# Kernel tuning notes

Hardware: AMD Instinct MI355X
Metric: run time of the kernel (lower is better)

The kernel has to match this reference:

```python
import jax, jax.numpy as jnp
import numpy as np
from jax import lax

B_SZ = 64
D_MODEL = 768
D_INNER = 1536   # expand * d_model
D_STATE = 16
D_CONV = 4
DT_RANK = 48     # ceil(768/16)
ROWS, COLS = 16, 16
L = ROWS * COLS
LN_EPS = 1e-5


def setup_inputs() -> dict:
    key = jax.random.key(0)
    ks = jax.random.split(key, 16)
    def nrm(k, shape, s):
        return jax.random.normal(k, shape, jnp.float32) * s
    # A_log init as in Mamba: log(arange(1..d_state)) tiled over d_inner
    A_log = jnp.log(jnp.tile(jnp.arange(1, D_STATE + 1, dtype=jnp.float32)[None, :], (D_INNER, 1)))
    # dt bias init: inverse-softplus of dt ~ LogUniform(1e-3, 1e-1)
    def dt_bias_init(k):
        u = jax.random.uniform(k, (D_INNER,), jnp.float32)
        dt = jnp.exp(u * (np.log(0.1) - np.log(0.001)) + np.log(0.001))
        return dt + jnp.log(-jnp.expm1(-dt))
    dt_std = DT_RANK ** -0.5
    return {
        "hidden_states": jax.random.normal(ks[0], (B_SZ, L, D_MODEL), jnp.float32),
        "in_proj_w": nrm(ks[1], (2 * D_INNER, D_MODEL), 0.02),
        "conv_w": nrm(ks[2], (D_INNER, D_CONV), 0.2),
        "conv_bias": nrm(ks[3], (D_INNER,), 0.1),
        "conv_w_b": nrm(ks[4], (D_INNER, D_CONV), 0.2),
        "conv_bias_b": nrm(ks[5], (D_INNER,), 0.1),
        "x_proj_w": nrm(ks[6], (DT_RANK + 2 * D_STATE, D_INNER), 0.02),
        "x_proj_w_b": nrm(ks[7], (DT_RANK + 2 * D_STATE, D_INNER), 0.02),
        "dt_proj_w": jax.random.uniform(ks[8], (D_INNER, DT_RANK), jnp.float32, -dt_std, dt_std),
        "dt_proj_w_b": jax.random.uniform(ks[9], (D_INNER, DT_RANK), jnp.float32, -dt_std, dt_std),
        "dt_bias": dt_bias_init(ks[10]),
        "dt_bias_b": dt_bias_init(ks[11]),
        "A_log": A_log,
        "A_b_log": A_log,
        "Dp": jnp.ones((D_INNER,), jnp.float32),
        "Dp_b": jnp.ones((D_INNER,), jnp.float32),
        "ln_gamma": jnp.ones((D_INNER,), jnp.float32),
        "ln_beta": jnp.zeros((D_INNER,), jnp.float32),
        "out_proj_w": nrm(ks[12], (D_MODEL, D_INNER), 0.02),
    }


def _causal_conv_silu(x, w, b):
    # x: (B, D, L); depthwise causal conv (left-pad K-1) + SiLU
    y = lax.conv_general_dilated(x, w[:, None, :], (1,), [(D_CONV - 1, 0)],
                                 dimension_numbers=("NCH", "OIH", "NCH"),
                                 feature_group_count=D_INNER)
    return jax.nn.silu(y + b[None, :, None])


def _selective_scan(u, dt, A_log, Bm, Cm, dt_bias):
    # u, dt: (B, D, Lr); Bm, Cm: (B, N, Lr)
    A = -jnp.exp(A_log)                                     # (D, N)
    delta = jax.nn.softplus(dt + dt_bias[None, :, None])    # (B, D, Lr)
    dA = jnp.exp(jnp.einsum("bdl,dn->lbdn", delta, A))     # (Lr, B, D, N)
    dBu = jnp.einsum("bdl,bnl,bdl->lbdn", delta, Bm, u)    # (Lr, B, D, N)
    C_l = jnp.moveaxis(Cm, -1, 0)                           # (Lr, B, N)
    def step(h, inp):
        dA_t, dBu_t, C_t = inp
        h = dA_t * h + dBu_t
        return h, jnp.einsum("bdn,bn->bd", h, C_t)
    h0 = jnp.zeros(dA.shape[1:], dA.dtype)
    _, ys = lax.scan(step, h0, (dA, dBu, C_l))
    return jnp.moveaxis(ys, 0, -1)                          # (B, D, Lr)


def _direction(x, conv_w, conv_bias, x_proj_w, dt_proj_w, dt_bias, A_log, Dp):
    xc = _causal_conv_silu(x, conv_w, conv_bias)            # (B, D, L)
    x_comp = xc.reshape(-1, D_INNER, ROWS, COLS).mean(axis=3)  # (B, D, ROWS)
    x_dbl = jnp.einsum("bdl,ed->ble", x_comp, x_proj_w)    # (B, ROWS, R+2N)
    dt, Bm, Cm = jnp.split(x_dbl, [DT_RANK, DT_RANK + D_STATE], axis=-1)
    dt = jnp.einsum("blr,dr->bdl", dt, dt_proj_w)          # (B, D, ROWS)
    Bm = jnp.moveaxis(Bm, 1, 2)                             # (B, N, ROWS)
    Cm = jnp.moveaxis(Cm, 1, 2)
    y = _selective_scan(x_comp, dt, A_log, Bm, Cm, dt_bias)
    return jnp.repeat(y, COLS, axis=2) + Dp[None, :, None] * xc  # (B, D, L)


def reference(hidden_states, in_proj_w, conv_w, conv_bias, conv_w_b, conv_bias_b,
              x_proj_w, x_proj_w_b, dt_proj_w, dt_proj_w_b, dt_bias, dt_bias_b,
              A_log, A_b_log, Dp, Dp_b, ln_gamma, ln_beta, out_proj_w):
    xz = jnp.einsum("bld,ed->bel", hidden_states, in_proj_w)  # (B, 2*Di, L)
    x, z = jnp.split(xz, 2, axis=1)
    out_f = _direction(x, conv_w, conv_bias, x_proj_w, dt_proj_w, dt_bias, A_log, Dp)
    out_b = _direction(x[:, :, ::-1], conv_w_b, conv_bias_b, x_proj_w_b, dt_proj_w_b, dt_bias_b, A_b_log, Dp_b)
    comb = jnp.moveaxis((out_f + out_b[:, :, ::-1]) * 0.5, 1, 2)  # (B, L, Di)
    mu = comb.mean(-1, keepdims=True)
    var = comb.var(-1, keepdims=True)
    normed = (comb - mu) * lax.rsqrt(var + LN_EPS) * ln_gamma + ln_beta
    gated = normed * jax.nn.silu(jnp.moveaxis(z, 1, 2))
    return jnp.einsum("bld,od->blo", gated, out_proj_w)       # (B, L, d_model)
```

## Files before the change

kernel.cpp:

```cpp
#include <hip/hip_runtime.h>
#include <cstdint>
#include <cstddef>

typedef __bf16 bf16_t;
typedef __attribute__((ext_vector_type(2))) __bf16 bf16x2;
typedef __attribute__((ext_vector_type(8))) __bf16 bf16x8;
typedef __attribute__((ext_vector_type(4))) float f32x4;

#define NB     64
#define LSEQ   256
#define DM     768
#define DI     1536
#define NSTATE 16
#define NROWS  16
#define RANK   48

#define BF16_PROBE 0x3F803F80u

__device__ __forceinline__ float bf2f(bf16_t v) { return (float)v; }

__device__ __forceinline__ float ldp(const void* p, size_t i, bool isbf) {
  return isbf ? (float)((const bf16_t*)p)[i] : ((const float*)p)[i];
}

__device__ __forceinline__ float silu_f(float x) {
  const float e = __expf(-fabsf(x));
  return (x >= 0.f) ? (x / (1.f + e)) : (x * e / (1.f + e));
}

__device__ __forceinline__ void async16(const bf16_t* g, bf16_t* l) {
  __builtin_amdgcn_global_load_lds(
      (const __attribute__((address_space(1))) void*)g,
      (__attribute__((address_space(3))) void*)l, 16, 0, 0);
}

__global__ __launch_bounds__(256) void cvt_kernel(
    const void* __restrict__ in, bf16_t* __restrict__ out, int n8,
    const uint32_t* __restrict__ probe)
{
  const int i = blockIdx.x * 256 + threadIdx.x;
  if (i >= n8) return;
  if (probe[0] == BF16_PROBE) {
    ((bf16x8*)out)[i] = ((const bf16x8*)in)[i];
  } else {
    const float* f = (const float*)in + (size_t)i * 8;
    f32x4 lo = *(const f32x4*)f, hi = *(const f32x4*)(f + 4);
    ((bf16x8*)out)[i] = (bf16x8){(bf16_t)lo.x, (bf16_t)lo.y, (bf16_t)lo.z, (bf16_t)lo.w,
                                 (bf16_t)hi.x, (bf16_t)hi.y, (bf16_t)hi.z, (bf16_t)hi.w};
  }
}

__global__ __launch_bounds__(256) void gemm_bt_kernel(
    const bf16_t* __restrict__ A, const bf16_t* __restrict__ B,
    void* __restrict__ C, int M, int N, int K, int cIsF32)
{
  __shared__ bf16_t As[128 * 64];
  __shared__ bf16_t Bs[128 * 64];
  const int tid  = threadIdx.x;
  const int wave = tid >> 6;
  const int lane = tid & 63;
  const size_t bm = (size_t)blockIdx.y * 128;
  const size_t bn = (size_t)blockIdx.x * 128;
  const int wm = (wave >> 1) * 64;
  const int wn = (wave & 1) * 64;

  const int src_rr  = lane >> 3;
  const int src_col = ((lane & 7) ^ src_rr) * 8;

  f32x4 acc[4][4];
#pragma unroll
  for (int i = 0; i < 4; i++)
#pragma unroll
    for (int j = 0; j < 4; j++) acc[i][j] = (f32x4){0.f, 0.f, 0.f, 0.f};

  for (int k0 = 0; k0 < K; k0 += 64) {
#pragma unroll
    for (int j = 0; j < 4; j++) {
      const int c = wave * 4 + j;
      const size_t row = c * 8 + src_rr;
      async16(A + (bm + row) * (size_t)K + k0 + src_col, &As[c * 512]);
      async16(B + (bn + row) * (size_t)K + k0 + src_col, &Bs[c * 512]);
    }
    __syncthreads();
#pragma unroll
    for (int s = 0; s < 2; s++) {
      const int r    = lane & 15;
      const int quad = lane >> 4;
      const int r7   = lane & 7;
      const int slot = ((s * 4 + quad) ^ r7) * 8;
      bf16x8 af[4], bfr[4];
#pragma unroll
      for (int mt = 0; mt < 4; mt++)
        af[mt] = *(const bf16x8*)&As[(wm + mt * 16 + r) * 64 + slot];
#pragma unroll
      for (int nt = 0; nt < 4; nt++)
        bfr[nt] = *(const bf16x8*)&Bs[(wn + nt * 16 + r) * 64 + slot];
#pragma unroll
      for (int mt = 0; mt < 4; mt++)
#pragma unroll
        for (int nt = 0; nt < 4; nt++)
          acc[mt][nt] = __builtin_amdgcn_mfma_f32_16x16x32_bf16(
              af[mt], bfr[nt], acc[mt][nt], 0, 0, 0);
    }
    __syncthreads();
  }

  const int col = lane & 15;
  const int rb  = (lane >> 4) * 4;
#pragma unroll
  for (int mt = 0; mt < 4; mt++)
#pragma unroll
    for (int nt = 0; nt < 4; nt++)
#pragma unroll
      for (int r = 0; r < 4; r++) {
        const size_t m = bm + wm + mt * 16 + rb + r;
        const size_t n = bn + wn + nt * 16 + col;
        const size_t ci = m * (size_t)N + n;
        if (cIsF32) ((float*)C)[ci] = acc[mt][nt][r];
        else        ((bf16_t*)C)[ci] = (bf16_t)acc[mt][nt][r];
      }
}

__global__ __launch_bounds__(256) void conv_kernel(
    const bf16_t* __restrict__ xz,
    const void* __restrict__ cw_f, const void* __restrict__ cb_f,
    const void* __restrict__ cw_b, const void* __restrict__ cb_b,
    bf16_t* __restrict__ xc_f, bf16_t* __restrict__ xc_b,
    float* __restrict__ comp_f, float* __restrict__ comp_b,
    const uint32_t* __restrict__ probe)
{
  const bool isbf = (probe[0] == BF16_PROBE);
  const int dir = blockIdx.y;
  int bi = blockIdx.x;
  const int chunk = bi & 3;
  bi >>= 2;
  const int b = bi / 3;
  const int pblk = bi % 3;
  const int d0 = (pblk * 256 + threadIdx.x) * 2;
  const void* cw = dir ? cw_b : cw_f;
  const void* cb = dir ? cb_b : cb_f;
  bf16_t* xc = dir ? xc_b : xc_f;
  float* comp = dir ? comp_b : comp_f;

  const float w00 = ldp(cw, d0 * 4 + 0, isbf), w01 = ldp(cw, d0 * 4 + 1, isbf),
              w02 = ldp(cw, d0 * 4 + 2, isbf), w03 = ldp(cw, d0 * 4 + 3, isbf);
  const float w10 = ldp(cw, (d0 + 1) * 4 + 0, isbf), w11 = ldp(cw, (d0 + 1) * 4 + 1, isbf),
              w12 = ldp(cw, (d0 + 1) * 4 + 2, isbf), w13 = ldp(cw, (d0 + 1) * 4 + 3, isbf);
  const float bias0 = ldp(cb, d0, isbf), bias1 = ldp(cb, d0 + 1, isbf);

  float a3 = 0.f, a2 = 0.f, a1 = 0.f;
  float c3 = 0.f, c2 = 0.f, c1 = 0.f;
  const int lr0 = chunk * 64;
  if (lr0 >= 3) {
#pragma unroll
    for (int i = 3; i >= 1; --i) {
      const int lrp = lr0 - i;
      const int l = dir ? (LSEQ - 1 - lrp) : lrp;
      bf16x2 xv = *(const bf16x2*)(xz + ((size_t)b * LSEQ + l) * (2 * DI) + d0);
      a3 = a2; a2 = a1; a1 = (float)xv.x;
      c3 = c2; c2 = c1; c1 = (float)xv.y;
    }
  }

  float s0 = 0.f, s1 = 0.f;
  for (int lr = lr0; lr < lr0 + 64; ++lr) {
    const int l = dir ? (LSEQ - 1 - lr) : lr;
    bf16x2 xv = *(const bf16x2*)(xz + ((size_t)b * LSEQ + l) * (2 * DI) + d0);
    const float x0 = (float)xv.x, x1 = (float)xv.y;
    float y0 = silu_f(bias0 + w00 * a3 + w01 * a2 + w02 * a1 + w03 * x0);
    float y1 = silu_f(bias1 + w10 * c3 + w11 * c2 + w12 * c1 + w13 * x1);
    a3 = a2; a2 = a1; a1 = x0;
    c3 = c2; c2 = c1; c1 = x1;
    *(bf16x2*)(xc + ((size_t)b * LSEQ + lr) * DI + d0) = (bf16x2){(bf16_t)y0, (bf16_t)y1};
    s0 += y0; s1 += y1;
    if ((lr & 15) == 15) {
      size_t ci = ((size_t)b * NROWS + (lr >> 4)) * DI + d0;
      comp[ci]     = s0 * (1.f / 16.f);
      comp[ci + 1] = s1 * (1.f / 16.f);
      s0 = 0.f; s1 = 0.f;
    }
  }
}

__global__ __launch_bounds__(256) void xproj_kernel(
    const float* __restrict__ comp_f, const float* __restrict__ comp_b,
    const void* __restrict__ w_f, const void* __restrict__ w_b,
    float* __restrict__ xd_f, float* __restrict__ xd_b,
    const uint32_t* __restrict__ probe)
{
  const bool isbf = (probe[0] == BF16_PROBE);
  const int dir = blockIdx.y;
  const int row = blockIdx.x;
  const float* comp = dir ? comp_b : comp_f;
  const void* W = dir ? w_b : w_f;
  float* out = dir ? xd_b : xd_f;

  __shared__ float xrow[DI];
  for (int i = threadIdx.x; i < DI; i += 256) xrow[i] = comp[(size_t)row * DI + i];
  __syncthreads();

  const int wave = threadIdx.x >> 6, lane = threadIdx.x & 63;
  for (int oo = 0; oo < 20; ++oo) {
    const int o = wave * 20 + oo;
    float s = 0.f;
#pragma unroll
    for (int j = 0; j < 24; ++j) {
      const int k = lane + 64 * j;
      s += xrow[k] * ldp(W, (size_t)o * DI + k, isbf);
    }
    for (int off = 32; off; off >>= 1) s += __shfl_down(s, off);
    if (lane == 0) out[(size_t)row * 80 + o] = s;
  }
}

__global__ __launch_bounds__(256) void scan_kernel(
    const float* __restrict__ xd_fg, const float* __restrict__ xd_bg,
    const float* comp_f, const float* comp_b,
    const void* __restrict__ dtw_f, const void* __restrict__ dtw_b,
    const void* __restrict__ dtb_f, const void* __restrict__ dtb_b,
    const void* __restrict__ Al_f, const void* __restrict__ Al_b,
    float* y_fg, float* y_bg,
    const uint32_t* __restrict__ probe)
{
  const bool isbf = (probe[0] == BF16_PROBE);
  const int dir = blockIdx.y;
  const int b = blockIdx.x / 6;
  const int d = (blockIdx.x % 6) * 256 + threadIdx.x;
  const float* xd_g = dir ? xd_bg : xd_fg;
  const float* comp = dir ? comp_b : comp_f;
  const void* dtw = dir ? dtw_b : dtw_f;
  const void* dtb = dir ? dtb_b : dtb_f;
  const void* Al  = dir ? Al_b : Al_f;
  float* y = dir ? y_bg : y_fg;

  __shared__ float xd[NROWS * 80];
  for (int i = threadIdx.x; i < NROWS * 80; i += 256) xd[i] = xd_g[(size_t)b * (NROWS * 80) + i];
  __syncthreads();

  float dt[NROWS];
#pragma unroll
  for (int l = 0; l < NROWS; l++) dt[l] = 0.f;
  for (int r = 0; r < RANK; r++) {
    const float w = ldp(dtw, (size_t)d * RANK + r, isbf);
#pragma unroll
    for (int l = 0; l < NROWS; l++) dt[l] += xd[l * 80 + r] * w;
  }

  float A[NSTATE];
#pragma unroll
  for (int n = 0; n < NSTATE; n++) A[n] = -__expf(ldp(Al, (size_t)d * NSTATE + n, isbf));
  const float bias = ldp(dtb, d, isbf);

  float h[NSTATE];
#pragma unroll
  for (int n = 0; n < NSTATE; n++) h[n] = 0.f;

  for (int l = 0; l < NROWS; l++) {
    const float u = comp[((size_t)b * NROWS + l) * DI + d];
    const float dv = dt[l] + bias;
    const float delta = (dv > 15.f) ? dv : log1pf(__expf(dv));
    const float du = delta * u;
    float yv = 0.f;
#pragma unroll
    for (int n = 0; n < NSTATE; n++) {
      const float hn = __expf(delta * A[n]) * h[n] + du * xd[l * 80 + RANK + n];
      h[n] = hn;
      yv += hn * xd[l * 80 + RANK + NSTATE + n];
    }
    y[((size_t)b * NROWS + l) * DI + d] = yv;
  }
}

__global__ __launch_bounds__(256) void combine_kernel(
    const float* __restrict__ y_f, const float* __restrict__ y_b,
    bf16_t* xcg_f,
    const bf16_t* __restrict__ xc_b,
    const bf16_t* __restrict__ xz,
    const void* __restrict__ Dp, const void* __restrict__ Dp_b,
    const void* __restrict__ gamma, const void* __restrict__ beta,
    const uint32_t* __restrict__ probe)
{
  const bool isbf = (probe[0] == BF16_PROBE);
  const int m = blockIdx.x;
  const int b = m >> 8, l = m & 255;
  const int lr = LSEQ - 1 - l;
  const int tid = threadIdx.x;

  float v[6];
  float sum = 0.f, sq = 0.f;
#pragma unroll
  for (int i = 0; i < 6; i++) {
    const int d = tid + i * 256;
    const float cf = bf2f(xcg_f[((size_t)b * LSEQ + l) * DI + d]);
    const float cb = bf2f(xc_b[((size_t)b * LSEQ + lr) * DI + d]);
    const float vf = y_f[((size_t)b * NROWS + (l >> 4)) * DI + d] + ldp(Dp, d, isbf) * cf;
    const float vb = y_b[((size_t)b * NROWS + (lr >> 4)) * DI + d] + ldp(Dp_b, d, isbf) * cb;
    const float c = 0.5f * (vf + vb);
    v[i] = c; sum += c; sq += c * c;
  }
  for (int off = 32; off; off >>= 1) {
    sum += __shfl_down(sum, off);
    sq  += __shfl_down(sq, off);
  }
  __shared__ float rs[4], rq[4];
  if ((tid & 63) == 0) { rs[tid >> 6] = sum; rq[tid >> 6] = sq; }
  __syncthreads();
  const float S  = rs[0] + rs[1] + rs[2] + rs[3];
  const float SQ = rq[0] + rq[1] + rq[2] + rq[3];
  const float mu = S * (1.f / (float)DI);
  const float var = fmaxf(SQ * (1.f / (float)DI) - mu * mu, 0.f);
  const float rstd = rsqrtf(var + 1e-5f);
#pragma unroll
  for (int i = 0; i < 6; i++) {
    const int d = tid + i * 256;
    const float nrm = (v[i] - mu) * rstd * ldp(gamma, d, isbf) + ldp(beta, d, isbf);
    const float z = bf2f(xz[((size_t)b * LSEQ + l) * (2 * DI) + DI + d]);
    xcg_f[(size_t)m * DI + d] = (bf16_t)(nrm * silu_f(z));
  }
}

extern "C" void kernel_launch(void* const* d_in, const int* in_sizes, int n_in,
                              void* d_out, int out_size, void* d_ws, size_t ws_size,
                              hipStream_t stream)
{
  (void)in_sizes; (void)n_in; (void)out_size; (void)ws_size;
  const void* H     = d_in[0];
  const void* Win   = d_in[1];
  const void* cw_f  = d_in[2];
  const void* cb_f  = d_in[3];
  const void* cw_b  = d_in[4];
  const void* cb_b  = d_in[5];
  const void* xpw_f = d_in[6];
  const void* xpw_b = d_in[7];
  const void* dtw_f = d_in[8];
  const void* dtw_b = d_in[9];
  const void* dtb_f = d_in[10];
  const void* dtb_b = d_in[11];
  const void* Al_f  = d_in[12];
  const void* Al_b  = d_in[13];
  const void* Dp    = d_in[14];
  const void* Dp_b  = d_in[15];
  const void* gam   = d_in[16];
  const void* bet   = d_in[17];
  const void* Wout  = d_in[18];
  const uint32_t* probe = (const uint32_t*)d_in[14];

  const size_t M = (size_t)NB * LSEQ;
  char* ws = (char*)d_ws;
  bf16_t* xz    = (bf16_t*)ws;  ws += M * (2 * DI) * sizeof(bf16_t);
  bf16_t* xc_f  = (bf16_t*)ws;  ws += M * DI * sizeof(bf16_t);
  bf16_t* xc_b  = (bf16_t*)ws;  ws += M * DI * sizeof(bf16_t);
  float* comp_f = (float*)ws;   ws += (size_t)NB * NROWS * DI * sizeof(float);
  float* comp_b = (float*)ws;   ws += (size_t)NB * NROWS * DI * sizeof(float);
  float* xd_f   = (float*)ws;   ws += (size_t)NB * NROWS * 80 * sizeof(float);
  float* xd_b   = (float*)ws;   ws += (size_t)NB * NROWS * 80 * sizeof(float);
  bf16_t* Hb    = (bf16_t*)ws;  ws += M * DM * sizeof(bf16_t);
  bf16_t* Winb  = (bf16_t*)ws;  ws += (size_t)(2 * DI) * DM * sizeof(bf16_t);
  bf16_t* Woutb = (bf16_t*)ws;  ws += (size_t)DM * DI * sizeof(bf16_t);

  cvt_kernel<<<(int)((M * DM / 8 + 255) / 256), 256, 0, stream>>>(H, Hb, (int)(M * DM / 8), probe);
  cvt_kernel<<<(2 * DI * DM / 8 + 255) / 256, 256, 0, stream>>>(Win, Winb, 2 * DI * DM / 8, probe);
  cvt_kernel<<<(DM * DI / 8 + 255) / 256, 256, 0, stream>>>(Wout, Woutb, DM * DI / 8, probe);

  gemm_bt_kernel<<<dim3(2 * DI / 128, M / 128), 256, 0, stream>>>(
      Hb, Winb, xz, (int)M, 2 * DI, DM, 0);

  conv_kernel<<<dim3(768, 2), 256, 0, stream>>>(
      xz, cw_f, cb_f, cw_b, cb_b, xc_f, xc_b, comp_f, comp_b, probe);

  xproj_kernel<<<dim3(NB * NROWS, 2), 256, 0, stream>>>(
      comp_f, comp_b, xpw_f, xpw_b, xd_f, xd_b, probe);

  scan_kernel<<<dim3(NB * (DI / 256), 2), 256, 0, stream>>>(
      xd_f, xd_b, comp_f, comp_b, dtw_f, dtw_b, dtb_f, dtb_b, Al_f, Al_b,
      comp_f, comp_b, probe);

  combine_kernel<<<dim3(NB * LSEQ), 256, 0, stream>>>(
      comp_f, comp_b, xc_f, xc_b, xz, Dp, Dp_b, gam, bet, probe);

  gemm_bt_kernel<<<dim3(DM / 128, M / 128), 256, 0, stream>>>(
      xc_f, Woutb, d_out, (int)M, DM, DI, 1);
}
```

Baseline: 517.0 us.

## Use 256x128 GEMM tile for in_proj, merge conv directions, vectorize combine

Adds a 256x128-tile GEMM for the input projection, doubling per-wave M work (8x4 MFMA tiles) to raise operand reuse from LDS and halve B-tile reloads. The conv kernel now handles both forward and backward directions in one block, reusing the same xz rows from cache instead of launching a second grid. The combine kernel switches to paired bf16x2/float2 loads and stores. The larger tile increases register pressure (128 accumulator floats per lane) and LDS use, and it halves the GEMM grid, which may reduce occupancy.

```diff
diff --git a/kernel.cpp b/kernel.cpp
--- a/kernel.cpp
+++ b/kernel.cpp
@@ -6,6 +6,7 @@
 typedef __attribute__((ext_vector_type(2))) __bf16 bf16x2;
 typedef __attribute__((ext_vector_type(8))) __bf16 bf16x8;
 typedef __attribute__((ext_vector_type(4))) float f32x4;
+typedef __attribute__((ext_vector_type(2))) float f32x2;
 
 #define NB     64
 #define LSEQ   256
@@ -85,9 +86,7 @@
 #pragma unroll
     for (int s = 0; s < 2; s++) {
       const int r    = lane & 15;
-      const int quad = lane >> 4;
-      const int r7   = lane & 7;
-      const int slot = ((s * 4 + quad) ^ r7) * 8;
+      const int slot = ((s * 4 + (lane >> 4)) ^ (lane & 7)) * 8;
       bf16x8 af[4], bfr[4];
 #pragma unroll
       for (int mt = 0; mt < 4; mt++)
@@ -118,6 +117,78 @@
         const size_t ci = m * (size_t)N + n;
         if (cIsF32) ((float*)C)[ci] = acc[mt][nt][r];
         else        ((bf16_t*)C)[ci] = (bf16_t)acc[mt][nt][r];
+      }
+}
+
+__global__ __launch_bounds__(256) void gemm_bt_256(
+    const bf16_t* __restrict__ A, const bf16_t* __restrict__ B,
+    bf16_t* __restrict__ C, int M, int N, int K)
+{
+  __shared__ bf16_t As[256 * 64];
+  __shared__ bf16_t Bs[128 * 64];
+  const int tid  = threadIdx.x;
+  const int wave = tid >> 6;
+  const int lane = tid & 63;
+  const size_t bm = (size_t)blockIdx.y * 256;
+  const size_t bn = (size_t)blockIdx.x * 128;
+  const int wm = (wave >> 1) * 128;
+  const int wn = (wave & 1) * 64;
+
+  const int src_rr  = lane >> 3;
+  const int src_col = ((lane & 7) ^ src_rr) * 8;
+
+  f32x4 acc[8][4];
+#pragma unroll
+  for (int i = 0; i < 8; i++)
+#pragma unroll
+    for (int j = 0; j < 4; j++) acc[i][j] = (f32x4){0.f, 0.f, 0.f, 0.f};
+
+  for (int k0 = 0; k0 < K; k0 += 64) {
+#pragma unroll
+    for (int j = 0; j < 8; j++) {
+      const int c = wave * 8 + j;
+      const size_t row = c * 8 + src_rr;
+      async16(A + (bm + row) * (size_t)K + k0 + src_col, &As[c * 512]);
+    }
+#pragma unroll
+    for (int j = 0; j < 4; j++) {
+      const int c = wave * 4 + j;
+      const size_t row = c * 8 + src_rr;
+      async16(B + (bn + row) * (size_t)K + k0 + src_col, &Bs[c * 512]);
+    }
+    __syncthreads();
+#pragma unroll
+    for (int s = 0; s < 2; s++) {
+      const int r    = lane & 15;
+      const int slot = ((s * 4 + (lane >> 4)) ^ (lane & 7)) * 8;
+      bf16x8 af[8], bfr[4];
+#pragma unroll
+      for (int mt = 0; mt < 8; mt++)
+        af[mt] = *(const bf16x8*)&As[(wm + mt * 16 + r) * 64 + slot];
+#pragma unroll
+      for (int nt = 0; nt < 4; nt++)
+        bfr[nt] = *(const bf16x8*)&Bs[(wn + nt * 16 + r) * 64 + slot];
+#pragma unroll
+      for (int mt = 0; mt < 8; mt++)
+#pragma unroll
+        for (int nt = 0; nt < 4; nt++)
+          acc[mt][nt] = __builtin_amdgcn_mfma_f32_16x16x32_bf16(
+              af[mt], bfr[nt], acc[mt][nt], 0, 0, 0);
+    }
+    __syncthreads();
+  }
+
+  const int col = lane & 15;
+  const int rb  = (lane >> 4) * 4;
+#pragma unroll
+  for (int mt = 0; mt < 8; mt++)
+#pragma unroll
+    for (int nt = 0; nt < 4; nt++)
+#pragma unroll
+      for (int r = 0; r < 4; r++) {
+        const size_t m = bm + wm + mt * 16 + rb + r;
+        const size_t n = bn + wn + nt * 16 + col;
+        C[m * (size_t)N + n] = (bf16_t)acc[mt][nt][r];
       }
 }
 
@@ -130,54 +201,83 @@
     const uint32_t* __restrict__ probe)
 {
   const bool isbf = (probe[0] == BF16_PROBE);
-  const int dir = blockIdx.y;
   int bi = blockIdx.x;
   const int chunk = bi & 3;
   bi >>= 2;
   const int b = bi / 3;
   const int pblk = bi % 3;
   const int d0 = (pblk * 256 + threadIdx.x) * 2;
-  const void* cw = dir ? cw_b : cw_f;
-  const void* cb = dir ? cb_b : cb_f;
-  bf16_t* xc = dir ? xc_b : xc_f;
-  float* comp = dir ? comp_b : comp_f;
-
-  const float w00 = ldp(cw, d0 * 4 + 0, isbf), w01 = ldp(cw, d0 * 4 + 1, isbf),
-              w02 = ldp(cw, d0 * 4 + 2, isbf), w03 = ldp(cw, d0 * 4 + 3, isbf);
-  const float w10 = ldp(cw, (d0 + 1) * 4 + 0, isbf), w11 = ldp(cw, (d0 + 1) * 4 + 1, isbf),
-              w12 = ldp(cw, (d0 + 1) * 4 + 2, isbf), w13 = ldp(cw, (d0 + 1) * 4 + 3, isbf);
-  const float bias0 = ldp(cb, d0, isbf), bias1 = ldp(cb, d0 + 1, isbf);
-
-  float a3 = 0.f, a2 = 0.f, a1 = 0.f;
-  float c3 = 0.f, c2 = 0.f, c1 = 0.f;
-  const int lr0 = chunk * 64;
-  if (lr0 >= 3) {
-#pragma unroll
-    for (int i = 3; i >= 1; --i) {
-      const int lrp = lr0 - i;
-      const int l = dir ? (LSEQ - 1 - lrp) : lrp;
-      bf16x2 xv = *(const bf16x2*)(xz + ((size_t)b * LSEQ + l) * (2 * DI) + d0);
-      a3 = a2; a2 = a1; a1 = (float)xv.x;
-      c3 = c2; c2 = c1; c1 = (float)xv.y;
-    }
-  }
-
-  float s0 = 0.f, s1 = 0.f;
-  for (int lr = lr0; lr < lr0 + 64; ++lr) {
-    const int l = dir ? (LSEQ - 1 - lr) : lr;
-    bf16x2 xv = *(const bf16x2*)(xz + ((size_t)b * LSEQ + l) * (2 * DI) + d0);
-    const float x0 = (float)xv.x, x1 = (float)xv.y;
-    float y0 = silu_f(bias0 + w00 * a3 + w01 * a2 + w02 * a1 + w03 * x0);
-    float y1 = silu_f(bias1 + w10 * c3 + w11 * c2 + w12 * c1 + w13 * x1);
-    a3 = a2; a2 = a1; a1 = x0;
-    c3 = c2; c2 = c1; c1 = x1;
-    *(bf16x2*)(xc + ((size_t)b * LSEQ + lr) * DI + d0) = (bf16x2){(bf16_t)y0, (bf16_t)y1};
-    s0 += y0; s1 += y1;
-    if ((lr & 15) == 15) {
-      size_t ci = ((size_t)b * NROWS + (lr >> 4)) * DI + d0;
-      comp[ci]     = s0 * (1.f / 16.f);
-      comp[ci + 1] = s1 * (1.f / 16.f);
-      s0 = 0.f; s1 = 0.f;
+
+  const float fw00 = ldp(cw_f, d0 * 4 + 0, isbf), fw01 = ldp(cw_f, d0 * 4 + 1, isbf),
+              fw02 = ldp(cw_f, d0 * 4 + 2, isbf), fw03 = ldp(cw_f, d0 * 4 + 3, isbf);
+  const float fw10 = ldp(cw_f, (d0 + 1) * 4 + 0, isbf), fw11 = ldp(cw_f, (d0 + 1) * 4 + 1, isbf),
+              fw12 = ldp(cw_f, (d0 + 1) * 4 + 2, isbf), fw13 = ldp(cw_f, (d0 + 1) * 4 + 3, isbf);
+  const float fb0 = ldp(cb_f, d0, isbf), fb1 = ldp(cb_f, d0 + 1, isbf);
+  const float bw00 = ldp(cw_b, d0 * 4 + 0, isbf), bw01 = ldp(cw_b, d0 * 4 + 1, isbf),
+              bw02 = ldp(cw_b, d0 * 4 + 2, isbf), bw03 = ldp(cw_b, d0 * 4 + 3, isbf);
+  const float bw10 = ldp(cw_b, (d0 + 1) * 4 + 0, isbf), bw11 = ldp(cw_b, (d0 + 1) * 4 + 1, isbf),
+              bw12 = ldp(cw_b, (d0 + 1) * 4 + 2, isbf), bw13 = ldp(cw_b, (d0 + 1) * 4 + 3, isbf);
+  const float bb0 = ldp(cb_b, d0, isbf), bb1 = ldp(cb_b, d0 + 1, isbf);
+
+  const size_t rowbase = (size_t)b * LSEQ;
+  const int l0 = chunk * 64;
+
+  {
+    float a3 = 0.f, a2 = 0.f, a1 = 0.f, c3 = 0.f, c2 = 0.f, c1 = 0.f;
+    if (l0 >= 3) {
+#pragma unroll
+      for (int i = 3; i >= 1; --i) {
+        bf16x2 xv = *(const bf16x2*)(xz + (rowbase + l0 - i) * (2 * DI) + d0);
+        a3 = a2; a2 = a1; a1 = (float)xv.x;
+        c3 = c2; c2 = c1; c1 = (float)xv.y;
+      }
+    }
+    float s0 = 0.f, s1 = 0.f;
+    for (int l = l0; l < l0 + 64; ++l) {
+      bf16x2 xv = *(const bf16x2*)(xz + (rowbase + l) * (2 * DI) + d0);
+      const float x0 = (float)xv.x, x1 = (float)xv.y;
+      float y0 = silu_f(fb0 + fw00 * a3 + fw01 * a2 + fw02 * a1 + fw03 * x0);
+      float y1 = silu_f(fb1 + fw10 * c3 + fw11 * c2 + fw12 * c1 + fw13 * x1);
+      a3 = a2; a2 = a1; a1 = x0;
+      c3 = c2; c2 = c1; c1 = x1;
+      *(bf16x2*)(xc_f + (rowbase + l) * DI + d0) = (bf16x2){(bf16_t)y0, (bf16_t)y1};
+      s0 += y0; s1 += y1;
+      if ((l & 15) == 15) {
+        size_t ci = ((size_t)b * NROWS + (l >> 4)) * DI + d0;
+        comp_f[ci]     = s0 * (1.f / 16.f);
+        comp_f[ci + 1] = s1 * (1.f / 16.f);
+        s0 = 0.f; s1 = 0.f;
+      }
+    }
+  }
+
+  {
+    float a3 = 0.f, a2 = 0.f, a1 = 0.f, c3 = 0.f, c2 = 0.f, c1 = 0.f;
+    if (chunk < 3) {
+#pragma unroll
+      for (int i = 3; i >= 1; --i) {
+        bf16x2 xv = *(const bf16x2*)(xz + (rowbase + l0 + 63 + i) * (2 * DI) + d0);
+        a3 = a2; a2 = a1; a1 = (float)xv.x;
+        c3 = c2; c2 = c1; c1 = (float)xv.y;
+      }
+    }
+    float s0 = 0.f, s1 = 0.f;
+    for (int s = l0 + 63; s >= l0; --s) {
+      const int lr = LSEQ - 1 - s;
+      bf16x2 xv = *(const bf16x2*)(xz + (rowbase + s) * (2 * DI) + d0);
+      const float x0 = (float)xv.x, x1 = (float)xv.y;
+      float y0 = silu_f(bb0 + bw00 * a3 + bw01 * a2 + bw02 * a1 + bw03 * x0);
+      float y1 = silu_f(bb1 + bw10 * c3 + bw11 * c2 + bw12 * c1 + bw13 * x1);
+      a3 = a2; a2 = a1; a1 = x0;
+      c3 = c2; c2 = c1; c1 = x1;
+      *(bf16x2*)(xc_b + (rowbase + lr) * DI + d0) = (bf16x2){(bf16_t)y0, (bf16_t)y1};
+      s0 += y0; s1 += y1;
+      if ((lr & 15) == 15) {
+        size_t ci = ((size_t)b * NROWS + (lr >> 4)) * DI + d0;
+        comp_b[ci]     = s0 * (1.f / 16.f);
+        comp_b[ci + 1] = s1 * (1.f / 16.f);
+        s0 = 0.f; s1 = 0.f;
+      }
     }
   }
 }
@@ -285,18 +385,26 @@
   const int b = m >> 8, l = m & 255;
   const int lr = LSEQ - 1 - l;
   const int tid = threadIdx.x;
+  const size_t rowF = ((size_t)b * LSEQ + l) * DI;
+  const size_t rowB = ((size_t)b * LSEQ + lr) * DI;
+  const size_t rowYF = ((size_t)b * NROWS + (l >> 4)) * DI;
+  const size_t rowYB = ((size_t)b * NROWS + (lr >> 4)) * DI;
 
   float v[6];
   float sum = 0.f, sq = 0.f;
 #pragma unroll
-  for (int i = 0; i < 6; i++) {
-    const int d = tid + i * 256;
-    const float cf = bf2f(xcg_f[((size_t)b * LSEQ + l) * DI + d]);
-    const float cb = bf2f(xc_b[((size_t)b * LSEQ + lr) * DI + d]);
-    const float vf = y_f[((size_t)b * NROWS + (l >> 4)) * DI + d] + ldp(Dp, d, isbf) * cf;
-    const float vb = y_b[((size_t)b * NROWS + (lr >> 4)) * DI + d] + ldp(Dp_b, d, isbf) * cb;
-    const float c = 0.5f * (vf + vb);
-    v[i] = c; sum += c; sq += c * c;
+  for (int i = 0; i < 3; i++) {
+    const int d = tid * 2 + i * 512;
+    bf16x2 cf2 = *(const bf16x2*)&xcg_f[rowF + d];
+    bf16x2 cb2 = *(const bf16x2*)&xc_b[rowB + d];
+    f32x2 yf2 = *(const f32x2*)&y_f[rowYF + d];
+    f32x2 yb2 = *(const f32x2*)&y_b[rowYB + d];
+    const float c0 = 0.5f * ((yf2.x + ldp(Dp, d, isbf) * (float)cf2.x) +
+                             (yb2.x + ldp(Dp_b, d, isbf) * (float)cb2.x));
+    const float c1 = 0.5f * ((yf2.y + ldp(Dp, d + 1, isbf) * (float)cf2.y) +
+                             (yb2.y + ldp(Dp_b, d + 1, isbf) * (float)cb2.y));
+    v[2 * i] = c0; v[2 * i + 1] = c1;
+    sum += c0 + c1; sq += c0 * c0 + c1 * c1;
   }
   for (int off = 32; off; off >>= 1) {
     sum += __shfl_down(sum, off);
@@ -311,11 +419,13 @@
   const float var = fmaxf(SQ * (1.f / (float)DI) - mu * mu, 0.f);
   const float rstd = rsqrtf(var + 1e-5f);
 #pragma unroll
-  for (int i = 0; i < 6; i++) {
-    const int d = tid + i * 256;
-    const float nrm = (v[i] - mu) * rstd * ldp(gamma, d, isbf) + ldp(beta, d, isbf);
-    const float z = bf2f(xz[((size_t)b * LSEQ + l) * (2 * DI) + DI + d]);
-    xcg_f[(size_t)m * DI + d] = (bf16_t)(nrm * silu_f(z));
+  for (int i = 0; i < 3; i++) {
+    const int d = tid * 2 + i * 512;
+    bf16x2 z2 = *(const bf16x2*)&xz[rowF * 2 + DI + d];
+    const float n0 = (v[2 * i] - mu) * rstd * ldp(gamma, d, isbf) + ldp(beta, d, isbf);
+    const float n1 = (v[2 * i + 1] - mu) * rstd * ldp(gamma, d + 1, isbf) + ldp(beta, d + 1, isbf);
+    *(bf16x2*)&xcg_f[(size_t)m * DI + d] =
+        (bf16x2){(bf16_t)(n0 * silu_f((float)z2.x)), (bf16_t)(n1 * silu_f((float)z2.y))};
   }
 }
 
@@ -362,10 +472,10 @@
   cvt_kernel<<<(2 * DI * DM / 8 + 255) / 256, 256, 0, stream>>>(Win, Winb, 2 * DI * DM / 8, probe);
   cvt_kernel<<<(DM * DI / 8 + 255) / 256, 256, 0, stream>>>(Wout, Woutb, DM * DI / 8, probe);
 
-  gemm_bt_kernel<<<dim3(2 * DI / 128, M / 128), 256, 0, stream>>>(
-      Hb, Winb, xz, (int)M, 2 * DI, DM, 0);
-
-  conv_kernel<<<dim3(768, 2), 256, 0, stream>>>(
+  gemm_bt_256<<<dim3(2 * DI / 128, M / 256), 256, 0, stream>>>(
+      Hb, Winb, xz, (int)M, 2 * DI, DM);
+
+  conv_kernel<<<dim3(768), 256, 0, stream>>>(
       xz, cw_f, cb_f, cw_b, cb_b, xc_f, xc_b, comp_f, comp_b, probe);
 
   xproj_kernel<<<dim3(NB * NROWS, 2), 256, 0, stream>>>(
```

Result: slower. 587.2 us (+13.6%).
